# Performance work log

Measured on AMD Instinct MI355X. Metric: run time of the kernel, lower is better.

The kernel has to match this reference:

```python
import jax, jax.numpy as jnp
import numpy as np

E, QE, P, H = 3, 60000, 40, 20   # elements, atoms per element, fp length, hidden
NIMG = 1800                       # images in batch
Q = E * QE                        # total atoms
NNZ = 14_400_000                  # nnz of sparse fprimes [P*Q, 3*Q]


def setup_inputs() -> dict:
    key = jax.random.key(0)
    ks = jax.random.split(key, 12)
    fps = jax.random.normal(ks[0], (E, QE, P), jnp.float32)
    image_idx = jax.random.randint(ks[1], (E, QE), 0, NIMG, jnp.int32)
    s1 = 1.0 / np.sqrt(P)
    s2 = 1.0 / np.sqrt(H)
    W1 = (jax.random.normal(ks[2], (E, P, H)) * s1).astype(jnp.float32)
    b1 = jnp.zeros((E, H), jnp.float32)
    W2 = (jax.random.normal(ks[3], (E, H, H)) * s2).astype(jnp.float32)
    b2 = jnp.zeros((E, H), jnp.float32)
    W3 = (jax.random.normal(ks[4], (E, H, 1)) * s2).astype(jnp.float32)
    b3 = jnp.zeros((E, 1), jnp.float32)
    fp_rows = jax.random.randint(ks[5], (NNZ,), 0, P * Q, jnp.int32)
    fp_cols = jax.random.randint(ks[6], (NNZ,), 0, 3 * Q, jnp.int32)
    fp_vals = (jax.random.normal(ks[7], (NNZ,)) * 0.05).astype(jnp.float32)
    return {"fps": fps, "W1": W1, "b1": b1, "W2": W2, "b2": b2, "W3": W3,
            "b3": b3, "image_idx": image_idx, "fp_rows": fp_rows,
            "fp_cols": fp_cols, "fp_vals": fp_vals, "batch_size": NIMG}


def _mlp(x, w1, b1, w2, b2, w3, b3):
    # Dense(tanh) -> Dense(tanh) -> Dense(linear), per amptorch MLP(n_layers=3)
    h = jnp.tanh(x @ w1 + b1)
    h = jnp.tanh(h @ w2 + b2)
    return h @ w3 + b3  # [..., 1]


def _esum(x, w1, b1, w2, b2, w3, b3):
    return _mlp(x, w1, b1, w2, b2, w3, b3).sum()


def reference(fps, W1, b1, W2, b2, W3, b3, image_idx, fp_rows, fp_cols,
              fp_vals, batch_size):
    # per-element atomwise energies: [E, QE, 1]
    atom_e = jax.vmap(_mlp)(fps, W1, b1, W2, b2, W3, b3)
    # scatter-add atomic energies into per-image energies (index_add_)
    energy_pred = jax.ops.segment_sum(
        atom_e.reshape(-1, 1), image_idx.reshape(-1).astype(jnp.int32),
        num_segments=batch_size)  # [NIMG, 1]
    # dE/dFP per atom (each atom's output depends only on its own fp, so
    # grad of the per-element energy sum == per-atom jacobian rows)
    dE_dFP = jax.vmap(jax.grad(_esum))(fps, W1, b1, W2, b2, W3, b3)  # [E,QE,P]
    # reorder atoms from element-grouped order to image-index order
    # (stable argsort == boolean-match reorder in the torch code)
    order = jnp.argsort(image_idx.reshape(-1))
    dE_flat = dE_dFP.reshape(-1, P)[order].reshape(-1)  # [P*Q]
    # force = -fprimes^T @ dE_dFP  (sparse COO matvec via segment_sum)
    force_flat = -jax.ops.segment_sum(
        fp_vals * dE_flat[fp_rows], fp_cols, num_segments=3 * Q)
    force_pred = force_flat.reshape(-1, 3)  # [Q, 3]
    return energy_pred, force_pred
```

## Files before the change

kernel.cpp:

```cpp
#include <hip/hip_runtime.h>
#include <math.h>

#define E_    3
#define QE_   60000
#define QTOT  180000
#define P_    40
#define H_    20
#define NIMG_ 1800
#define NNZ_  14400000
#define BLK   256
#define NB    704

#define CW_BITS 12
#define CW      4096
#define NBIN    132
#define SUBS    8
#define SC      8192
#define NSB     1758

#define SLICE_SHIFT 17
#define NSLICE  55
#define CAPS    270336
#define CAPB    114688

#define SCF     4096
#define NCHMAX  512
#define FS_GRID 1792
#define FS_PERX 224

#define C_SCUR  0
#define C_BCUR  64
#define C_GCNT  256
#define C_GRP   512
#define C_INTS  4608

typedef int   vi4 __attribute__((ext_vector_type(4)));
typedef float vf4 __attribute__((ext_vector_type(4)));
typedef unsigned uint32;

__global__ void zero_kernel(float* __restrict__ out, int n) {
    int i = blockIdx.x * blockDim.x + threadIdx.x;
    if (i < n) out[i] = 0.0f;
}
__global__ void zero_ctrl_kernel(int* __restrict__ ctrl) {
    ctrl[threadIdx.x] = 0;
}

__global__ void hist_kernel(const int* __restrict__ img, int* __restrict__ g_hist) {
    __shared__ int h[NIMG_];
    const int t = threadIdx.x, b = blockIdx.x;
    for (int v = t; v < NIMG_; v += BLK) h[v] = 0;
    __syncthreads();
    int a = b * BLK + t;
    if (a < QTOT) atomicAdd(&h[img[a]], 1);
    __syncthreads();
    for (int v = t; v < NIMG_; v += BLK) g_hist[v * NB + b] = h[v];
}

__global__ void scan_blocks_kernel(int* __restrict__ g_hist, int* __restrict__ g_total) {
    __shared__ int s[BLK];
    const int v = blockIdx.x, t = threadIdx.x;
    int carry = 0;
    for (int c = 0; c < NB; c += BLK) {
        int idx = c + t;
        int val = (idx < NB) ? g_hist[v * NB + idx] : 0;
        s[t] = val; __syncthreads();
        for (int off = 1; off < BLK; off <<= 1) {
            int tmp = (t >= off) ? s[t - off] : 0;
            __syncthreads();
            s[t] += tmp;
            __syncthreads();
        }
        int excl = s[t] - val;
        int tot  = s[BLK - 1];
        if (idx < NB) g_hist[v * NB + idx] = carry + excl;
        carry += tot;
        __syncthreads();
    }
    if (t == 0) g_total[v] = carry;
}

__global__ void scan_buckets_kernel(const int* __restrict__ g_total, int* __restrict__ g_base) {
    __shared__ int s[BLK];
    const int t = threadIdx.x;
    int carry = 0;
    for (int c = 0; c < NIMG_; c += BLK) {
        int idx = c + t;
        int val = (idx < NIMG_) ? g_total[idx] : 0;
        s[t] = val; __syncthreads();
        for (int off = 1; off < BLK; off <<= 1) {
            int tmp = (t >= off) ? s[t - off] : 0;
            __syncthreads();
            s[t] += tmp;
            __syncthreads();
        }
        if (idx < NIMG_) g_base[idx] = carry + (s[t] - val);
        carry += s[BLK - 1];
        __syncthreads();
    }
}

__global__ void rank_kernel(const int* __restrict__ img, const int* __restrict__ g_hist,
                            const int* __restrict__ g_base, int* __restrict__ rank) {
    __shared__ int simg[BLK];
    const int t = threadIdx.x, b = blockIdx.x;
    int a = b * BLK + t;
    int v = (a < QTOT) ? img[a] : -1;
    simg[t] = v;
    __syncthreads();
    if (a < QTOT) {
        int local = 0;
        for (int j = 0; j < t; ++j) {
            if (simg[j] == v) local++;
        }
        rank[a] = g_base[v] + g_hist[v * NB + b] + local;
    }
}

__global__ __launch_bounds__(BLK) void mlp_kernel(
    const float* __restrict__ fps, const float* __restrict__ W1, const float* __restrict__ b1,
    const float* __restrict__ W2, const float* __restrict__ b2, const float* __restrict__ W3,
    const float* __restrict__ b3, const int* __restrict__ img, const int* __restrict__ rank,
    float* __restrict__ energy, float* __restrict__ dEflat)
{
    __shared__ float sW1[P_ * H_], sW2[H_ * H_], sW3[H_], sB1[H_], sB2[H_];
    __shared__ float sB3;
    const int e = blockIdx.y;
    const int t = threadIdx.x;
    for (int i = t; i < P_ * H_; i += BLK) sW1[i] = W1[e * P_ * H_ + i];
    for (int i = t; i < H_ * H_; i += BLK) sW2[i] = W2[e * H_ * H_ + i];
    if (t < H_) { sW3[t] = W3[e * H_ + t]; sB1[t] = b1[e * H_ + t]; sB2[t] = b2[e * H_ + t]; }
    if (t == 0) sB3 = b3[e];
    __syncthreads();

    int q = blockIdx.x * BLK + t;
    if (q >= QE_) return;
    int a = e * QE_ + q;

    const vf4* xp = (const vf4*)(fps + (size_t)a * P_);
    float x[P_];
    #pragma unroll
    for (int p = 0; p < P_; p += 4) {
        vf4 v4 = __builtin_nontemporal_load(xp + (p >> 2));
        x[p] = v4.x; x[p+1] = v4.y; x[p+2] = v4.z; x[p+3] = v4.w;
    }

    float h1v[H_], h2v[H_];
    #pragma unroll
    for (int i = 0; i < H_; ++i) {
        float z = sB1[i];
        #pragma unroll
        for (int p = 0; p < P_; ++p) z += x[p] * sW1[p * H_ + i];
        h1v[i] = tanhf(z);
    }
    #pragma unroll
    for (int i = 0; i < H_; ++i) {
        float z = sB2[i];
        #pragma unroll
        for (int j = 0; j < H_; ++j) z += h1v[j] * sW2[j * H_ + i];
        h2v[i] = tanhf(z);
    }
    float ea = sB3;
    #pragma unroll
    for (int i = 0; i < H_; ++i) ea += h2v[i] * sW3[i];
    atomicAdd(&energy[img[a]], ea);

    float dz2[H_];
    #pragma unroll
    for (int i = 0; i < H_; ++i) dz2[i] = sW3[i] * (1.0f - h2v[i] * h2v[i]);
    float dz1[H_];
    #pragma unroll
    for (int i = 0; i < H_; ++i) {
        float d = 0.0f;
        #pragma unroll
        for (int j = 0; j < H_; ++j) d += sW2[i * H_ + j] * dz2[j];
        dz1[i] = d * (1.0f - h1v[i] * h1v[i]);
    }
    float* op = dEflat + (size_t)rank[a] * P_;
    #pragma unroll
    for (int p = 0; p < P_; p += 4) {
        float4 v4;
        float d0 = 0.f, d1 = 0.f, d2 = 0.f, d3 = 0.f;
        #pragma unroll
        for (int i = 0; i < H_; ++i) {
            d0 += sW1[(p    ) * H_ + i] * dz1[i];
            d1 += sW1[(p + 1) * H_ + i] * dz1[i];
            d2 += sW1[(p + 2) * H_ + i] * dz1[i];
            d3 += sW1[(p + 3) * H_ + i] * dz1[i];
        }
        v4.x = d0; v4.y = d1; v4.z = d2; v4.w = d3;
        *(float4*)(op + p) = v4;
    }
}


__global__ __launch_bounds__(BLK) void slice_scatter_kernel(
    const int* __restrict__ rows, const int* __restrict__ cols, const float* __restrict__ vals,
    int* __restrict__ ctrl, uint2* __restrict__ items)
{
    __shared__ uint32 srow[SC];
    __shared__ int h[NSLICE], lcur[NSLICE], gbase[NSLICE];
    const int t = threadIdx.x, b = blockIdx.x;
    const int base = b * SC;
    const int len = min(SC, NNZ_ - base);
    const bool full = (len == SC);

    if (t < NSLICE) h[t] = 0;
    __syncthreads();
    if (full) {
        const vi4* r4 = (const vi4*)(rows + base);
        #pragma unroll
        for (int j = 0; j < SC / (BLK * 4); ++j) {
            int idx = j * BLK + t;
            vi4 rr = __builtin_nontemporal_load(r4 + idx);
            srow[idx * 4 + 0] = (uint32)rr.x; atomicAdd(&h[rr.x >> SLICE_SHIFT], 1);
            srow[idx * 4 + 1] = (uint32)rr.y; atomicAdd(&h[rr.y >> SLICE_SHIFT], 1);
            srow[idx * 4 + 2] = (uint32)rr.z; atomicAdd(&h[rr.z >> SLICE_SHIFT], 1);
            srow[idx * 4 + 3] = (uint32)rr.w; atomicAdd(&h[rr.w >> SLICE_SHIFT], 1);
        }
    } else {
        for (int j = t; j < len; j += BLK) {
            int r = rows[base + j];
            srow[j] = (uint32)r;
            atomicAdd(&h[r >> SLICE_SHIFT], 1);
        }
    }
    __syncthreads();
    if (t < NSLICE) {
        lcur[t] = 0;
        gbase[t] = (h[t] > 0) ? atomicAdd(&ctrl[C_SCUR + t], h[t]) : 0;
    }
    __syncthreads();
    if (full) {
        const vi4* c4 = (const vi4*)(cols + base);
        const vi4* v4 = (const vi4*)(vals + base);
        #pragma unroll 2
        for (int j = 0; j < SC / (BLK * 4); ++j) {
            int idx = j * BLK + t;
            vi4 cc = __builtin_nontemporal_load(c4 + idx);
            vi4 vv = __builtin_nontemporal_load(v4 + idx);
            #define EMIT(K, CI, VB)                                                \
            {                                                                      \
                uint32 r = srow[idx * 4 + K];                                      \
                int sl = (int)(r >> SLICE_SHIFT);                                  \
                int pos = gbase[sl] + atomicAdd(&lcur[sl], 1);                     \
                uint32 v15 = (((uint32)(VB)) + 0x10000u) >> 17;                    \
                items[(size_t)sl * CAPS + pos] =                                   \
                    make_uint2((v15 << 17) | (r & 0x1FFFFu), (uint32)(CI));        \
            }
            EMIT(0, cc.x, vv.x)
            EMIT(1, cc.y, vv.y)
            EMIT(2, cc.z, vv.z)
            EMIT(3, cc.w, vv.w)
        }
    } else {
        for (int j = t; j < len; j += BLK) {
            uint32 r = srow[j];
            int sl = (int)(r >> SLICE_SHIFT);
            int pos = gbase[sl] + atomicAdd(&lcur[sl], 1);
            uint32 vb = ((const uint32*)vals)[base + j];
            uint32 v15 = (vb + 0x10000u) >> 17;
            items[(size_t)sl * CAPS + pos] =
                make_uint2((v15 << 17) | (r & 0x1FFFFu), (uint32)cols[base + j]);
        }
    }
}

__global__ void plan4_kernel(int* __restrict__ ctrl) {
    __shared__ int scnt[NSLICE], cb[NSLICE + 1], gp[NSLICE];
    __shared__ int g8[8], tot_s;
    const int t = threadIdx.x;
    if (t < NSLICE) scnt[t] = ctrl[C_SCUR + t];
    __syncthreads();
    if (t == 0) {
        int crun = 0;
        int gs[8]; for (int x = 0; x < 8; ++x) gs[x] = 0;
        for (int s = 0; s < NSLICE; ++s) {
            int nc = (scnt[s] + SCF - 1) / SCF;
            cb[s] = crun; crun += nc;
            int x = s & 7;
            gp[s] = gs[x]; gs[x] += nc;
        }
        cb[NSLICE] = crun; tot_s = crun;
        for (int x = 0; x < 8; ++x) g8[x] = gs[x];
    }
    __syncthreads();
    const int tot = tot_s;
    if (t < 8) ctrl[C_GCNT + t] = g8[t];
    for (int idx = t; idx < tot; idx += BLK) {
        int s = 0;
        for (int k = 0; k < NSLICE; ++k) if (cb[k] <= idx) s = k;
        int c = idx - cb[s];
        ctrl[C_GRP + (s & 7) * NCHMAX + gp[s] + c] = (s << 8) | c;
    }
}

__global__ __launch_bounds__(BLK) void fscatter4_kernel(
    const uint2* __restrict__ items, const float* __restrict__ dEflat,
    int* __restrict__ ctrl, uint32* __restrict__ bm)
{
    __shared__ uint32 itl[SCF];
    __shared__ int h[NBIN], cur[NBIN], ls[NBIN], dlt[NBIN];
    __shared__ int sc[BLK];
    const int t = threadIdx.x;
    const int x = blockIdx.x & 7;
    const int r = blockIdx.x >> 3;
    const int gc = ctrl[C_GCNT + x];

    for (int w = r; w < gc; w += FS_PERX) {
        const int pkd   = ctrl[C_GRP + x * NCHMAX + w];
        const int sl    = pkd >> 8;
        const int c     = pkd & 255;
        const int start = sl * CAPS + c * SCF;
        const int len   = min(SCF, ctrl[C_SCUR + sl] - c * SCF);
        const float* __restrict__ dE = dEflat + ((size_t)sl << SLICE_SHIFT);

        if (t < NBIN) h[t] = 0;
        __syncthreads();
        if (len == SCF) {
            const vi4* p4 = (const vi4*)(items + start);
            #pragma unroll
            for (int j = 0; j < SCF / (BLK * 2); ++j) {
                vi4 q = __builtin_nontemporal_load(p4 + j * BLK + t);
                atomicAdd(&h[((uint32)q.y) >> CW_BITS], 1);
                atomicAdd(&h[((uint32)q.w) >> CW_BITS], 1);
            }
        } else {
            for (int j = t; j < len; j += BLK)
                atomicAdd(&h[items[start + j].y >> CW_BITS], 1);
        }
        __syncthreads();
        {
            int v = (t < NBIN) ? h[t] : 0;
            sc[t] = v; __syncthreads();
            for (int off = 1; off < BLK; off <<= 1) {
                int tmp = (t >= off) ? sc[t - off] : 0;
                __syncthreads();
                sc[t] += tmp;
                __syncthreads();
            }
            if (t < NBIN) {
                int st = sc[t] - v;
                ls[t] = st;
                cur[t] = st;
                int gb = (v > 0) ? atomicAdd(&ctrl[C_BCUR + t], v) : 0;
                dlt[t] = t * CAPB + gb;
            }
        }
        __syncthreads();
        #define PLACE4(LO, CO, DI)                                             \
        {                                                                      \
            uint32 col = (uint32)(CO);                                         \
            int bin = (int)(col >> CW_BITS);                                   \
            float val = __uint_as_float((((uint32)(LO)) >> 17) << 17);         \
            uint32 u = __float_as_uint(-val * (DI));                           \
            uint32 pk = ((col & (CW - 1)) << 20) | ((u + 0x800u) >> 12);       \
            int pos = atomicAdd(&cur[bin], 1);                                 \
            itl[pos] = pk;                                                     \
        }
        if (len == SCF) {
            const vi4* p4 = (const vi4*)(items + start);
            #pragma unroll 4
            for (int j = 0; j < SCF / (BLK * 2); ++j) {
                vi4 q = __builtin_nontemporal_load(p4 + j * BLK + t);
                float dA = dE[((uint32)q.x) & 0x1FFFFu];
                float dB = dE[((uint32)q.z) & 0x1FFFFu];
                PLACE4(q.x, q.y, dA)
                PLACE4(q.z, q.w, dB)
            }
        } else {
            for (int j = t; j < len; j += BLK) {
                uint2 it = items[start + j];
                float d = dE[it.x & 0x1FFFFu];
                PLACE4(it.x, it.y, d)
            }
        }
        __syncthreads();
        {
            const int wv = t >> 6, ln = t & 63;
            for (int b = wv; b < NBIN; b += 4) {
                int s0 = ls[b];
                int cnt = cur[b] - s0;
                int gb = dlt[b];
                for (int k = ln; k < cnt; k += 64)
                    __builtin_nontemporal_store(itl[s0 + k], &bm[gb + k]);
            }
        }
        __syncthreads();
    }
}

__global__ __launch_bounds__(BLK) void fforce4_kernel(
    const uint32* __restrict__ bm, const int* __restrict__ ctrl,
    float* __restrict__ partial)
{
    __shared__ float w[CW];
    const int t = threadIdx.x;
    const int bin = blockIdx.x >> 3;
    const int sub = blockIdx.x & (SUBS - 1);
    for (int i = t; i < CW; i += BLK) w[i] = 0.0f;
    __syncthreads();
    const int cnt   = ctrl[C_BCUR + bin];
    const int start = bin * CAPB;
    const int sBeg  = start + (cnt * sub) / SUBS;
    const int sEnd  = start + (cnt * (sub + 1)) / SUBS;
    int i = sBeg + t;
    for (; i + 3 * BLK < sEnd; i += 4 * BLK) {
        uint32 p0 = __builtin_nontemporal_load(bm + i);
        uint32 p1 = __builtin_nontemporal_load(bm + i + BLK);
        uint32 p2 = __builtin_nontemporal_load(bm + i + 2 * BLK);
        uint32 p3 = __builtin_nontemporal_load(bm + i + 3 * BLK);
        atomicAdd(&w[p0 >> 20], __uint_as_float((p0 & 0xFFFFFu) << 12));
        atomicAdd(&w[p1 >> 20], __uint_as_float((p1 & 0xFFFFFu) << 12));
        atomicAdd(&w[p2 >> 20], __uint_as_float((p2 & 0xFFFFFu) << 12));
        atomicAdd(&w[p3 >> 20], __uint_as_float((p3 & 0xFFFFFu) << 12));
    }
    for (; i < sEnd; i += BLK) {
        uint32 p = bm[i];
        atomicAdd(&w[p >> 20], __uint_as_float((p & 0xFFFFFu) << 12));
    }
    __syncthreads();
    float* dst = partial + (size_t)blockIdx.x * CW;
    for (int k = t; k < CW; k += BLK) __builtin_nontemporal_store(w[k], dst + k);
}

__global__ void freduce_kernel(const float* __restrict__ partial, float* __restrict__ force) {
    int i = blockIdx.x * BLK + threadIdx.x;
    if (i < 3 * QTOT) {
        int bin = i >> CW_BITS, local = i & (CW - 1);
        const float* p = partial + (size_t)bin * (CW * SUBS) + local;
        float sum = 0.0f;
        #pragma unroll
        for (int k = 0; k < SUBS; ++k) sum += __builtin_nontemporal_load(p + k * CW);
        force[i] = sum;
    }
}

__global__ __launch_bounds__(BLK) void fhist_kernel(const int* __restrict__ cols,
                                                    int* __restrict__ binHist) {
    __shared__ int h[NBIN];
    const int t = threadIdx.x, b = blockIdx.x;
    if (t < NBIN) h[t] = 0;
    __syncthreads();
    const int base = b * SC;
    if (base + SC <= NNZ_) {
        const vi4* c4 = (const vi4*)(cols + base);
        #pragma unroll
        for (int j = 0; j < SC / (BLK * 4); ++j) {
            vi4 cc = __builtin_nontemporal_load(c4 + j * BLK + t);
            atomicAdd(&h[cc.x >> CW_BITS], 1);
            atomicAdd(&h[cc.y >> CW_BITS], 1);
            atomicAdd(&h[cc.z >> CW_BITS], 1);
            atomicAdd(&h[cc.w >> CW_BITS], 1);
        }
    } else {
        for (int j = 0; j < SC / BLK; ++j) {
            int k = base + j * BLK + t;
            if (k < NNZ_) atomicAdd(&h[cols[k] >> CW_BITS], 1);
        }
    }
    __syncthreads();
    if (t < NBIN) binHist[t * NSB + b] = h[t];
}

__global__ void fscan_blocks_kernel(int* __restrict__ binHist, int* __restrict__ binTotal,
                                    int n) {
    __shared__ int s[BLK];
    const int v = blockIdx.x, t = threadIdx.x;
    int carry = 0;
    for (int c = 0; c < n; c += BLK) {
        int idx = c + t;
        int val = (idx < n) ? binHist[v * n + idx] : 0;
        s[t] = val; __syncthreads();
        for (int off = 1; off < BLK; off <<= 1) {
            int tmp = (t >= off) ? s[t - off] : 0;
            __syncthreads();
            s[t] += tmp;
            __syncthreads();
        }
        int excl = s[t] - val;
        int tot  = s[BLK - 1];
        if (idx < n) binHist[v * n + idx] = carry + excl;
        carry += tot;
        __syncthreads();
    }
    if (t == 0) binTotal[v] = carry;
}

__global__ void fbase_kernel(const int* __restrict__ binTotal, int* __restrict__ binBase) {
    __shared__ int s[BLK];
    const int t = threadIdx.x;
    int v = (t < NBIN) ? binTotal[t] : 0;
    s[t] = v; __syncthreads();
    for (int off = 1; off < BLK; off <<= 1) {
        int tmp = (t >= off) ? s[t - off] : 0;
        __syncthreads();
        s[t] += tmp;
        __syncthreads();
    }
    if (t < NBIN) binBase[t] = s[t] - v;
    if (t == 0) binBase[NBIN] = s[BLK - 1];
}

__global__ __launch_bounds__(BLK) void fscatter_kernel(
    const int* __restrict__ rows, const int* __restrict__ cols, const float* __restrict__ vals,
    const float* __restrict__ dEflat, const int* __restrict__ binHist,
    const int* __restrict__ binBase, uint32* __restrict__ bm)
{
    __shared__ uint32 items[SC];
    __shared__ unsigned char bins[SC];
    __shared__ int hist[NBIN];
    __shared__ int cursor[NBIN];
    __shared__ int delta[NBIN];
    __shared__ int s[BLK];
    const int t = threadIdx.x, b = blockIdx.x;
    const int base = b * SC;
    const int nIt = min(SC, NNZ_ - base);
    const bool full = (base + SC <= NNZ_);

    if (t < NBIN) hist[t] = 0;
    __syncthreads();
    if (full) {
        const vi4* c4 = (const vi4*)(cols + base);
        #pragma unroll
        for (int j = 0; j < SC / (BLK * 4); ++j) {
            vi4 cc = __builtin_nontemporal_load(c4 + j * BLK + t);
            atomicAdd(&hist[cc.x >> CW_BITS], 1);
            atomicAdd(&hist[cc.y >> CW_BITS], 1);
            atomicAdd(&hist[cc.z >> CW_BITS], 1);
            atomicAdd(&hist[cc.w >> CW_BITS], 1);
        }
    } else {
        for (int j = 0; j < SC / BLK; ++j) {
            int k = base + j * BLK + t;
            if (k < NNZ_) atomicAdd(&hist[cols[k] >> CW_BITS], 1);
        }
    }
    __syncthreads();
    {
        int v = (t < NBIN) ? hist[t] : 0;
        s[t] = v; __syncthreads();
        for (int off = 1; off < BLK; off <<= 1) {
            int tmp = (t >= off) ? s[t - off] : 0;
            __syncthreads();
            s[t] += tmp;
            __syncthreads();
        }
        if (t < NBIN) {
            int ls = s[t] - v;
            cursor[t] = ls;
            delta[t]  = binBase[t] + binHist[t * NSB + b] - ls;
        }
    }
    __syncthreads();
    if (full) {
        const vi4* c4 = (const vi4*)(cols + base);
        const vi4* r4 = (const vi4*)(rows + base);
        const vf4* v4 = (const vf4*)(vals + base);
        #pragma unroll 2
        for (int j = 0; j < SC / (BLK * 4); ++j) {
            int idx = j * BLK + t;
            vi4 cc = __builtin_nontemporal_load(c4 + idx);
            vi4 rr = __builtin_nontemporal_load(r4 + idx);
            vf4 vv = __builtin_nontemporal_load(v4 + idx);
            float d0 = dEflat[rr.x];
            float d1 = dEflat[rr.y];
            float d2 = dEflat[rr.z];
            float d3 = dEflat[rr.w];
            #define PLACE(CI, VI, DI)                                              \
            {                                                                      \
                int bin = (CI) >> CW_BITS;                                         \
                uint32 u = __float_as_uint(-(VI) * (DI));                          \
                uint32 pk = ((uint32)((CI) & (CW - 1)) << 20)                      \
                            | ((u + 0x800u) >> 12);                                \
                int pos = atomicAdd(&cursor[bin], 1);                              \
                items[pos] = pk;                                                   \
                bins[pos] = (unsigned char)bin;                                    \
            }
            PLACE(cc.x, vv.x, d0)
            PLACE(cc.y, vv.y, d1)
            PLACE(cc.z, vv.z, d2)
            PLACE(cc.w, vv.w, d3)
        }
    } else {
        for (int j = 0; j < SC / BLK; ++j) {
            int k = base + j * BLK + t;
            if (k < NNZ_) {
                int c = cols[k];
                float d = dEflat[rows[k]];
                float v = vals[k];
                PLACE(c, v, d)
            }
        }
    }
    __syncthreads();
    for (int i = t; i < nIt; i += BLK) {
        __builtin_nontemporal_store(items[i], &bm[delta[bins[i]] + i]);
    }
}

__global__ __launch_bounds__(BLK) void fforce_kernel(
    const uint32* __restrict__ bm, const int* __restrict__ binBase,
    float* __restrict__ partial)
{
    __shared__ float w[CW];
    const int t = threadIdx.x;
    const int bin = blockIdx.x >> 3;
    const int sub = blockIdx.x & (SUBS - 1);
    for (int i = t; i < CW; i += BLK) w[i] = 0.0f;
    __syncthreads();
    const int start = binBase[bin];
    const int cnt   = binBase[bin + 1] - start;
    const int sBeg  = start + (cnt * sub) / SUBS;
    const int sEnd  = start + (cnt * (sub + 1)) / SUBS;
    int i = sBeg + t;
    for (; i + 3 * BLK < sEnd; i += 4 * BLK) {
        uint32 p0 = __builtin_nontemporal_load(bm + i);
        uint32 p1 = __builtin_nontemporal_load(bm + i + BLK);
        uint32 p2 = __builtin_nontemporal_load(bm + i + 2 * BLK);
        uint32 p3 = __builtin_nontemporal_load(bm + i + 3 * BLK);
        atomicAdd(&w[p0 >> 20], __uint_as_float((p0 & 0xFFFFFu) << 12));
        atomicAdd(&w[p1 >> 20], __uint_as_float((p1 & 0xFFFFFu) << 12));
        atomicAdd(&w[p2 >> 20], __uint_as_float((p2 & 0xFFFFFu) << 12));
        atomicAdd(&w[p3 >> 20], __uint_as_float((p3 & 0xFFFFFu) << 12));
    }
    for (; i < sEnd; i += BLK) {
        uint32 p = bm[i];
        atomicAdd(&w[p >> 20], __uint_as_float((p & 0xFFFFFu) << 12));
    }
    __syncthreads();
    float* dst = partial + (size_t)blockIdx.x * CW;
    for (int k = t; k < CW; k += BLK) __builtin_nontemporal_store(w[k], dst + k);
}

__global__ void force_kernel(const int* __restrict__ rows, const int* __restrict__ cols,
                             const float* __restrict__ vals, const float* __restrict__ dEflat,
                             float* __restrict__ force) {
    int k = blockIdx.x * blockDim.x + threadIdx.x;
    if (k < NNZ_) {
        float contrib = -vals[k] * dEflat[rows[k]];
        atomicAdd(&force[cols[k]], contrib);
    }
}

extern "C" void kernel_launch(void* const* d_in, const int* in_sizes, int n_in,
                              void* d_out, int out_size, void* d_ws, size_t ws_size,
                              hipStream_t stream) {
    (void)in_sizes; (void)n_in; (void)out_size;
    const float* fps  = (const float*)d_in[0];
    const float* W1   = (const float*)d_in[1];
    const float* b1   = (const float*)d_in[2];
    const float* W2   = (const float*)d_in[3];
    const float* b2   = (const float*)d_in[4];
    const float* W3   = (const float*)d_in[5];
    const float* b3   = (const float*)d_in[6];
    const int*   img  = (const int*)d_in[7];
    const int*   rows = (const int*)d_in[8];
    const int*   cols = (const int*)d_in[9];
    const float* vals = (const float*)d_in[10];

    char* ws = (char*)d_ws;
    float* energy = (float*)d_out;
    float* force  = (float*)d_out + NIMG_;
    const int nOut = NIMG_ + 3 * QTOT;

    int*    g_hist  = (int*)(ws);
    int*    g_total = (int*)(ws + 5068800);
    int*    g_base  = (int*)(ws + 5076000);
    int*    rank    = (int*)(ws + 5083200);
    uint2*  items   = (uint2*)(ws);
    float*  partial4= (float*)(ws);
    uint32* bm4     = (uint32*)(ws + 118947840);
    int*    ctrl    = (int*)(ws + 179503104);
    float*  dEflat4 = (float*)(ws + 179536384);
    const size_t WS_V4 = 208336384;

    float*  dEflat5   = (float*)(ws + 5803200);
    int*    binHist5  = (int*)(ws + 34603200);
    int*    binTotal5 = (int*)(ws + 35531424);
    int*    binBase5  = (int*)(ws + 35531952);
    uint32* bm5       = (uint32*)(ws + 35532496);
    float*  partial5  = (float*)(ws + 93132496);
    const size_t WS_V2 = 110434000;

    const bool v4 = (ws_size >= WS_V4);
    float* dEflat = v4 ? dEflat4 : dEflat5;

    zero_kernel<<<(nOut + BLK - 1) / BLK, BLK, 0, stream>>>((float*)d_out, nOut);

    hist_kernel<<<NB, BLK, 0, stream>>>(img, g_hist);
    scan_blocks_kernel<<<NIMG_, BLK, 0, stream>>>(g_hist, g_total);
    scan_buckets_kernel<<<1, BLK, 0, stream>>>(g_total, g_base);
    rank_kernel<<<NB, BLK, 0, stream>>>(img, g_hist, g_base, rank);

    dim3 gm((QE_ + BLK - 1) / BLK, E_);
    mlp_kernel<<<gm, BLK, 0, stream>>>(fps, W1, b1, W2, b2, W3, b3, img, rank,
                                       energy, dEflat);

    if (v4) {
        zero_ctrl_kernel<<<1, 256, 0, stream>>>(ctrl);
        slice_scatter_kernel<<<NSB, BLK, 0, stream>>>(rows, cols, vals, ctrl, items);
        plan4_kernel<<<1, BLK, 0, stream>>>(ctrl);
        fscatter4_kernel<<<FS_GRID, BLK, 0, stream>>>(items, dEflat, ctrl, bm4);
        fforce4_kernel<<<NBIN * SUBS, BLK, 0, stream>>>(bm4, ctrl, partial4);
        freduce_kernel<<<(3 * QTOT + BLK - 1) / BLK, BLK, 0, stream>>>(partial4, force);
    } else if (ws_size >= WS_V2) {
        fhist_kernel<<<NSB, BLK, 0, stream>>>(cols, binHist5);
        fscan_blocks_kernel<<<NBIN, BLK, 0, stream>>>(binHist5, binTotal5, NSB);
        fbase_kernel<<<1, BLK, 0, stream>>>(binTotal5, binBase5);
        fscatter_kernel<<<NSB, BLK, 0, stream>>>(rows, cols, vals, dEflat,
                                                 binHist5, binBase5, bm5);
        fforce_kernel<<<NBIN * SUBS, BLK, 0, stream>>>(bm5, binBase5, partial5);
        freduce_kernel<<<(3 * QTOT + BLK - 1) / BLK, BLK, 0, stream>>>(partial5, force);
    } else {
        force_kernel<<<NNZ_ / BLK, BLK, 0, stream>>>(rows, cols, vals, dEflat, force);
    }
}
```

Measured before the change: 628.8 us.

## Scatter packed force items directly to global bins, dropping LDS staging and scan

The fscatter kernel no longer stages items in a shared-memory buffer sorted by a block-wide prefix scan. Each item is written straight to its global bin slot using a per-bin shared atomic offset, and the chunk size doubles. This removes the log-step scan with its many barriers, the LDS staging and the separate copy-out pass, and cuts shared-memory use. In exchange the global writes become scattered rather than coalesced per bin. The larger chunk also changes how many chunks fit per slice, since the chunk grouping elsewhere depends on SCF.

```diff
diff --git a/kernel.cpp b/kernel.cpp
--- a/kernel.cpp
+++ b/kernel.cpp
@@ -23,7 +23,7 @@
 #define CAPS    270336
 #define CAPB    114688
 
-#define SCF     4096
+#define SCF     8192
 #define NCHMAX  512
 #define FS_GRID 1792
 #define FS_PERX 224
@@ -299,9 +299,8 @@
     const uint2* __restrict__ items, const float* __restrict__ dEflat,
     int* __restrict__ ctrl, uint32* __restrict__ bm)
 {
-    __shared__ uint32 itl[SCF];
-    __shared__ int h[NBIN], cur[NBIN], ls[NBIN], dlt[NBIN];
-    __shared__ int sc[BLK];
+    __shared__ int h[NBIN];
+    __shared__ int dlt[NBIN];
     const int t = threadIdx.x;
     const int x = blockIdx.x & 7;
     const int r = blockIdx.x >> 3;
@@ -330,22 +329,11 @@
                 atomicAdd(&h[items[start + j].y >> CW_BITS], 1);
         }
         __syncthreads();
-        {
-            int v = (t < NBIN) ? h[t] : 0;
-            sc[t] = v; __syncthreads();
-            for (int off = 1; off < BLK; off <<= 1) {
-                int tmp = (t >= off) ? sc[t - off] : 0;
-                __syncthreads();
-                sc[t] += tmp;
-                __syncthreads();
-            }
-            if (t < NBIN) {
-                int st = sc[t] - v;
-                ls[t] = st;
-                cur[t] = st;
-                int gb = (v > 0) ? atomicAdd(&ctrl[C_BCUR + t], v) : 0;
-                dlt[t] = t * CAPB + gb;
-            }
+        if (t < NBIN) {
+            int v = h[t];
+            int gb = (v > 0) ? atomicAdd(&ctrl[C_BCUR + t], v) : 0;
+            dlt[t] = t * CAPB + gb;
+            h[t] = 0;
         }
         __syncthreads();
         #define PLACE4(LO, CO, DI)                                             \
@@ -355,8 +343,8 @@
             float val = __uint_as_float((((uint32)(LO)) >> 17) << 17);         \
             uint32 u = __float_as_uint(-val * (DI));                           \
             uint32 pk = ((col & (CW - 1)) << 20) | ((u + 0x800u) >> 12);       \
-            int pos = atomicAdd(&cur[bin], 1);                                 \
-            itl[pos] = pk;                                                     \
+            int pos = atomicAdd(&h[bin], 1);                                   \
+            bm[dlt[bin] + pos] = pk;                                           \
         }
         if (len == SCF) {
             const vi4* p4 = (const vi4*)(items + start);
@@ -373,17 +361,6 @@
                 uint2 it = items[start + j];
                 float d = dE[it.x & 0x1FFFFu];
                 PLACE4(it.x, it.y, d)
-            }
-        }
-        __syncthreads();
-        {
-            const int wv = t >> 6, ln = t & 63;
-            for (int b = wv; b < NBIN; b += 4) {
-                int s0 = ls[b];
-                int cnt = cur[b] - s0;
-                int gb = dlt[b];
-                for (int k = ln; k < cnt; k += 64)
-                    __builtin_nontemporal_store(itl[s0 + k], &bm[gb + k]);
             }
         }
         __syncthreads();
```

New measurement: 787.2 us. 25.2% more time.
